# Kernel tuning notes

Measured on AMD Instinct MI355X. Metric: run time of the kernel, lower is better.

Reference implementation:

```python
import jax, jax.numpy as jnp
import numpy as np

B, L, D_MODEL, HEADS, EXP, DEPTH = 2, 2048, 1024, 16, 2, 12
D_EXP = D_MODEL * EXP
D_HEAD = D_EXP // HEADS


def _layernorm(x, g, b, eps=1e-5):
    mu = jnp.mean(x, axis=-1, keepdims=True)
    var = jnp.mean(jnp.square(x - mu), axis=-1, keepdims=True)
    return (x - mu) * jax.lax.rsqrt(var + eps) * g + b


def setup_inputs() -> dict:
    key = jax.random.key(0)
    ks = jax.random.split(key, 4)
    x = jax.random.normal(ks[0], (B, L, D_MODEL), dtype=jnp.float32)
    w_in = jax.random.normal(ks[1], (D_MODEL, 4 * D_EXP), dtype=jnp.float32) * 0.02
    w_out = jax.random.normal(ks[2], (D_EXP, D_MODEL), dtype=jnp.float32) * (0.02 / np.sqrt(2 * DEPTH))
    return {
        "x": x,
        "ln1_g": jnp.ones((D_MODEL,), jnp.float32),
        "ln1_b": jnp.zeros((D_MODEL,), jnp.float32),
        "ln2_g": jnp.ones((D_MODEL,), jnp.float32),
        "ln2_b": jnp.zeros((D_MODEL,), jnp.float32),
        "w_in": w_in,
        "w_out": w_out,
        "smear_factor": jnp.linspace(-6.0, 6.0, HEADS, dtype=jnp.float32),
        "log_scale": jnp.zeros((HEADS,), jnp.float32),
    }


def reference(x, ln1_g, ln1_b, ln2_g, ln2_b, w_in, w_out, smear_factor, log_scale):
    b, l, d = x.shape
    h = smear_factor.shape[0]
    d_exp = w_in.shape[1] // 4
    dh = d_exp // h

    qkvp = _layernorm(x, ln1_g, ln1_b) @ w_in  # [b, l, 4*d_exp]
    q, k, v, p = jnp.split(qkvp, 4, axis=-1)
    # 'b i (h d) -> b h i d'
    to_heads = lambda t: t.reshape(b, l, h, dh).transpose(0, 2, 1, 3)
    q, k, v = to_heads(q), to_heads(k), to_heads(v)

    # smeared keys: k_i <- (1-s)*k_i + s*k_{i-1}  (zero at i=0)
    smear = jax.nn.sigmoid(smear_factor)[None, :, None, None]
    k_prev = jnp.pad(k, ((0, 0), (0, 0), (1, 0), (0, 0)))[:, :, :-1, :]
    k = (1.0 - smear) * k + smear * k_prev

    # ALiBi-style additive mask: slope[h]*j on causal part, -1e10 above diag
    half = h // 2
    slopes = jnp.concatenate([2.0 ** jnp.linspace(0.0, -8.0, half), jnp.zeros((h - half,), jnp.float32)])
    j = jnp.arange(l)
    causal = jnp.where(j[None, :] > j[:, None], jnp.float32(-1e10), jnp.float32(0.0))  # [l, l]
    mask = slopes[:, None, None] * j[None, None, :].astype(jnp.float32) + causal[None, :, :]  # [h, l, l]

    # SDPA with q/s, k/s and default scale 1/sqrt(dh): logits = q k^T / (s^2 sqrt(dh))
    inv = 1.0 / (jnp.exp(2.0 * log_scale)[None, :, None, None] * jnp.sqrt(jnp.float32(dh)))
    logits = jnp.einsum('bhid,bhjd->bhij', q, k) * inv + mask[None]
    attn = jax.nn.softmax(logits, axis=-1)
    o = jnp.einsum('bhij,bhjd->bhid', attn, v)
    o = o.transpose(0, 2, 1, 3).reshape(b, l, h * dh)  # 'b h i d -> b i (h d)'

    out = (jax.nn.silu(p) * o) @ w_out
    return _layernorm(out, ln2_g, ln2_b)
```

## Files before the change

### kernel.cpp

```cpp
#include <hip/hip_runtime.h>

typedef unsigned short u16;
typedef __attribute__((ext_vector_type(8))) short bf16x8;
typedef __attribute__((ext_vector_type(8))) unsigned short u16x8;
typedef __attribute__((ext_vector_type(4))) float f32x4;

#define L_SEQ 2048
#define NTOK 4096
#define DMODEL 1024
#define DEXP 2048
#define NH 16
#define DH 128

__device__ __forceinline__ u16 f2bf(float f) {
    unsigned u = __float_as_uint(f);
    unsigned r = (u + 0x7FFFu + ((u >> 16) & 1u)) >> 16;
    return (u16)r;
}
__device__ __forceinline__ float bf2f(u16 h) {
    return __uint_as_float(((unsigned)h) << 16);
}

__device__ __forceinline__ void gl_lds16(const u16* g, u16* l) {
    __builtin_amdgcn_global_load_lds((const __attribute__((address_space(1))) void*)g,
                                     (__attribute__((address_space(3))) void*)l, 16, 0, 0);
}

__global__ void conv_transpose(const float* __restrict__ in, u16* __restrict__ out, int R, int C) {
    __shared__ unsigned tile[32][33];
    int c0 = blockIdx.x * 32, r0 = blockIdx.y * 32;
    int tx = threadIdx.x, ty = threadIdx.y;
    for (int j = 0; j < 32; j += 8)
        tile[ty + j][tx] = (unsigned)f2bf(in[(size_t)(r0 + ty + j) * C + c0 + tx]);
    __syncthreads();
    for (int j = 0; j < 32; j += 8)
        out[(size_t)(c0 + ty + j) * R + r0 + tx] = (u16)tile[tx][ty + j];
}

__global__ __launch_bounds__(256) void ln_fwd(const float* __restrict__ x, const float* __restrict__ g,
                                              const float* __restrict__ bta, void* __restrict__ outp,
                                              int out_bf16) {
    int row = blockIdx.x;
    int t = threadIdx.x;
    const float* xr = x + (size_t)row * DMODEL;
    float4 xv = *(const float4*)&xr[t * 4];
    float s = xv.x + xv.y + xv.z + xv.w;
    float s2 = xv.x * xv.x + xv.y * xv.y + xv.z * xv.z + xv.w * xv.w;
    for (int off = 32; off >= 1; off >>= 1) {
        s += __shfl_xor(s, off);
        s2 += __shfl_xor(s2, off);
    }
    __shared__ float red[10];
    int w = t >> 6;
    if ((t & 63) == 0) { red[w] = s; red[4 + w] = s2; }
    __syncthreads();
    if (t == 0) {
        red[8] = red[0] + red[1] + red[2] + red[3];
        red[9] = red[4] + red[5] + red[6] + red[7];
    }
    __syncthreads();
    float mu = red[8] * (1.0f / DMODEL);
    float var = red[9] * (1.0f / DMODEL) - mu * mu;
    float rstd = rsqrtf(var + 1e-5f);
    float vals[4] = {xv.x, xv.y, xv.z, xv.w};
    for (int e = 0; e < 4; e++) {
        int c = t * 4 + e;
        float y = (vals[e] - mu) * rstd * g[c] + bta[c];
        if (out_bf16) ((u16*)outp)[(size_t)row * DMODEL + c] = f2bf(y);
        else          ((float*)outp)[(size_t)row * DMODEL + c] = y;
    }
}

__device__ __forceinline__ void store_out(u16* C, size_t idx, float v) { C[idx] = f2bf(v); }
__device__ __forceinline__ void store_out(float* C, size_t idx, float v) { C[idx] = v; }

template <typename OutT>
__global__ __launch_bounds__(256) void gemm_bt(const u16* __restrict__ A, const u16* __restrict__ BT,
                                               OutT* __restrict__ C, int M, int N, int K) {
    __shared__ u16 a_s[2][4096];
    __shared__ u16 b_s[2][4096];
    int tid = threadIdx.x;
    unsigned NX = gridDim.x;
    unsigned lin = blockIdx.x + NX * blockIdx.y;
    unsigned per = NX >> 3;
    unsigned xcd = lin & 7, t = lin >> 3;
    unsigned n_p = xcd * per + (t % per);
    unsigned m_p = t / per;
    int m0 = m_p * 128, n0 = n_p * 128;
    int w = tid >> 6, lane = tid & 63, quad = lane >> 4, ln = lane & 15;
    int wr = (w >> 1) * 64, wc = (w & 1) * 64;
    f32x4 zero4 = {0.f, 0.f, 0.f, 0.f};
    f32x4 acc[4][4];
    for (int r = 0; r < 4; r++)
        for (int c = 0; c < 4; c++) acc[r][c] = zero4;

    int lrow = lane >> 2;
    int lseg = ((lane & 3) ^ ((lrow >> 1) & 3)) * 8;
    int qsw = (quad ^ ((ln >> 1) & 3)) * 8;
    const u16* Ag0 = A + (size_t)(m0 + 32 * w + lrow) * K + lseg;
    const u16* Ag1 = Ag0 + (size_t)16 * K;
    const u16* Bg0 = BT + (size_t)(n0 + 32 * w + lrow) * K + lseg;
    const u16* Bg1 = Bg0 + (size_t)16 * K;
    int lo0 = (2 * w) * 512, lo1 = (2 * w + 1) * 512;

    gl_lds16(Ag0, &a_s[0][lo0]);
    gl_lds16(Ag1, &a_s[0][lo1]);
    gl_lds16(Bg0, &b_s[0][lo0]);
    gl_lds16(Bg1, &b_s[0][lo1]);
    __syncthreads();

    int cur = 0;
    for (int k0 = 0; k0 < K; k0 += 32) {
        if (k0 + 32 < K) {
            int nb = cur ^ 1;
            gl_lds16(Ag0 + k0 + 32, &a_s[nb][lo0]);
            gl_lds16(Ag1 + k0 + 32, &a_s[nb][lo1]);
            gl_lds16(Bg0 + k0 + 32, &b_s[nb][lo0]);
            gl_lds16(Bg1 + k0 + 32, &b_s[nb][lo1]);
        }
        bf16x8 af[4], bfr[4];
        for (int r = 0; r < 4; r++) af[r]  = *(const bf16x8*)&a_s[cur][(wr + r * 16 + ln) * 32 + qsw];
        for (int c = 0; c < 4; c++) bfr[c] = *(const bf16x8*)&b_s[cur][(wc + c * 16 + ln) * 32 + qsw];
        __builtin_amdgcn_s_setprio(1);
        for (int r = 0; r < 4; r++)
            for (int c = 0; c < 4; c++)
                acc[r][c] = __builtin_amdgcn_mfma_f32_16x16x32_bf16(af[r], bfr[c], acc[r][c], 0, 0, 0);
        __builtin_amdgcn_s_setprio(0);
        __syncthreads();
        cur ^= 1;
    }
    for (int r = 0; r < 4; r++)
        for (int c = 0; c < 4; c++)
            for (int e = 0; e < 4; e++) {
                int row = m0 + wr + r * 16 + quad * 4 + e;
                int col = n0 + wc + c * 16 + ln;
                store_out(C, (size_t)row * N + col, acc[r][c][e]);
            }
}

__global__ __launch_bounds__(256) void gemm_bt64(const u16* __restrict__ A, const u16* __restrict__ BT,
                                                 float* __restrict__ C, int M, int N, int K) {
    __shared__ u16 a_s[2][2048];
    __shared__ u16 b_s[2][4096];
    int tid = threadIdx.x;
    unsigned NX = gridDim.x;
    unsigned lin = blockIdx.x + NX * blockIdx.y;
    unsigned per = NX >> 3;
    unsigned xcd = lin & 7, t = lin >> 3;
    unsigned n_p = xcd * per + (t % per);
    unsigned m_p = t / per;
    int m0 = m_p * 64, n0 = n_p * 128;
    int w = tid >> 6, lane = tid & 63, quad = lane >> 4, ln = lane & 15;
    int wc = w * 32;
    f32x4 zero4 = {0.f, 0.f, 0.f, 0.f};
    f32x4 acc[4][2];
    for (int r = 0; r < 4; r++)
        for (int c = 0; c < 2; c++) acc[r][c] = zero4;

    int lrow = lane >> 2;
    int lseg = ((lane & 3) ^ ((lrow >> 1) & 3)) * 8;
    int qsw = (quad ^ ((ln >> 1) & 3)) * 8;
    const u16* Ag  = A + (size_t)(m0 + 16 * w + lrow) * K + lseg;
    const u16* Bg0 = BT + (size_t)(n0 + 32 * w + lrow) * K + lseg;
    const u16* Bg1 = Bg0 + (size_t)16 * K;
    int la = w * 512;
    int lb0 = (2 * w) * 512, lb1 = (2 * w + 1) * 512;

    gl_lds16(Ag, &a_s[0][la]);
    gl_lds16(Bg0, &b_s[0][lb0]);
    gl_lds16(Bg1, &b_s[0][lb1]);
    __syncthreads();

    int cur = 0;
    for (int k0 = 0; k0 < K; k0 += 32) {
        if (k0 + 32 < K) {
            int nb = cur ^ 1;
            gl_lds16(Ag + k0 + 32, &a_s[nb][la]);
            gl_lds16(Bg0 + k0 + 32, &b_s[nb][lb0]);
            gl_lds16(Bg1 + k0 + 32, &b_s[nb][lb1]);
        }
        bf16x8 af[4], bfr[2];
        for (int r = 0; r < 4; r++) af[r]  = *(const bf16x8*)&a_s[cur][(r * 16 + ln) * 32 + qsw];
        for (int c = 0; c < 2; c++) bfr[c] = *(const bf16x8*)&b_s[cur][(wc + c * 16 + ln) * 32 + qsw];
        __builtin_amdgcn_s_setprio(1);
        for (int r = 0; r < 4; r++)
            for (int c = 0; c < 2; c++)
                acc[r][c] = __builtin_amdgcn_mfma_f32_16x16x32_bf16(af[r], bfr[c], acc[r][c], 0, 0, 0);
        __builtin_amdgcn_s_setprio(0);
        __syncthreads();
        cur ^= 1;
    }
    for (int r = 0; r < 4; r++)
        for (int c = 0; c < 2; c++)
            for (int e = 0; e < 4; e++) {
                int row = m0 + r * 16 + quad * 4 + e;
                int col = n0 + wc + c * 16 + ln;
                C[(size_t)row * N + col] = acc[r][c][e];
            }
}

__global__ __launch_bounds__(256) void smear_kernel(const u16* __restrict__ qkvp,
                                                    const float* __restrict__ smear_f,
                                                    u16* __restrict__ k_sm) {
    int gid = blockIdx.x * 256 + threadIdx.x;
    int base = gid * 8;
    int bl = base >> 11;
    int c = base & 2047;
    int h = c >> 7;
    int d = c & 127;
    int l = bl & (L_SEQ - 1);
    int bb = bl >> 11;
    float s = 1.0f / (1.0f + __expf(-smear_f[h]));
    u16x8 cur = *(const u16x8*)&qkvp[(size_t)bl * 8192 + 2048 + c];
    u16x8 prv = {0, 0, 0, 0, 0, 0, 0, 0};
    if (l > 0) prv = *(const u16x8*)&qkvp[(size_t)(bl - 1) * 8192 + 2048 + c];
    u16x8 outv;
    for (int u = 0; u < 8; u++) {
        float kc = bf2f(cur[u]);
        float kp = bf2f(prv[u]);
        outv[u] = f2bf((1.0f - s) * kc + s * kp);
    }
    *(u16x8*)&k_sm[(((size_t)(bb * 16 + h)) * L_SEQ + l) * DH + d] = outv;
}

__global__ void vT_kernel(const u16* __restrict__ qkvp, u16* __restrict__ v_t) {
    __shared__ unsigned tile[32][33];
    int l0 = blockIdx.x * 32, d0 = blockIdx.y * 32;
    int bh = blockIdx.z;
    int bb = bh >> 4, h = bh & 15;
    int tx = threadIdx.x, ty = threadIdx.y;
    size_t tokb = (size_t)bb * L_SEQ;
    for (int j = 0; j < 32; j += 8)
        tile[ty + j][tx] = (unsigned)qkvp[(tokb + l0 + ty + j) * 8192 + 4096 + h * DH + d0 + tx];
    __syncthreads();
    for (int j = 0; j < 32; j += 8)
        v_t[((size_t)bh * DH + d0 + ty + j) * L_SEQ + l0 + tx] = (u16)tile[tx][ty + j];
}

__global__ __launch_bounds__(256) void attn_kernel(const u16* __restrict__ qkvp,
                                                   const u16* __restrict__ k_sm,
                                                   const u16* __restrict__ v_t,
                                                   u16* __restrict__ ag2,
                                                   const float* __restrict__ log_scale) {
    __shared__ u16 k_s[16384];
    __shared__ u16 vt_s[16384];
    __shared__ u16 p_s[4608];
    int tid = threadIdx.x;
    unsigned lin = blockIdx.x + 16u * blockIdx.y;
    unsigned xcd = lin & 7, tt = lin >> 3;
    int bh = (int)(xcd * 4 + (tt & 3));
    int pair = (int)(tt >> 2);
    int bb = bh >> 4, h = bh & 15;
    int w = tid >> 6, lane = tid & 63, quad = lane >> 4, ln = lane & 15;
    size_t tokb = (size_t)bb * L_SEQ;

    const float LOG2E = 1.44269504f;
    float inv = 1.0f / (__expf(2.0f * log_scale[h]) * sqrtf((float)DH));
    float scl = inv * LOG2E;
    float slope2 = ((h < 8) ? exp2f(-8.0f * (float)h / 7.0f) : 0.0f) * LOG2E;

    int lrow = lane >> 2, lcol = lane & 3;
    int lsw8 = (lcol ^ ((lrow >> 1) & 3)) * 8;
    int qsw = (quad ^ ((ln >> 1) & 3)) * 8;
    f32x4 zero4 = {0.f, 0.f, 0.f, 0.f};
    u16* pw = &p_s[w * 1152];
    const short ONE_BF = (short)0x3F80;
    bf16x8 ones = {ONE_BF, ONE_BF, ONE_BF, ONE_BF, ONE_BF, ONE_BF, ONE_BF, ONE_BF};

    for (int sidx = 0; sidx < 2; sidx++) {
        int ib = sidx == 0 ? (31 - pair) : pair;
        int i0 = ib * 64;
        int si = i0 + w * 16;
        int iq = si + ln;

        bf16x8 qf[4];
        for (int kt = 0; kt < 4; kt++)
            qf[kt] = *(const bf16x8*)&qkvp[(tokb + si + ln) * 8192 + h * DH + kt * 32 + quad * 8];

        float mshift = -1e30f;
        float astep = slope2 * 64.0f;
        f32x4 o_acc[8], l_acc;
        for (int dt = 0; dt < 8; dt++) o_acc[dt] = zero4;
        l_acc = zero4;

        float adt0[4][4];
        for (int ct = 0; ct < 4; ct++)
            for (int r = 0; r < 4; r++)
                adt0[ct][r] = slope2 * (float)(ct * 16 + quad * 4 + r);

        const u16* kg[4];
        for (int g = 0; g < 4; g++)
            kg[g] = k_sm + ((size_t)bh * L_SEQ + g * 16 + lrow) * DH + w * 32 + lsw8;
        const u16* vg[4];
        int vloff[4];
        for (int q = 0; q < 4; q++) {
            int c = w * 4 + q;
            int jt = c >> 3, dg = c & 7;
            vg[q] = v_t + ((size_t)bh * DH + dg * 16 + lrow) * L_SEQ + jt * 32 + lsw8;
            vloff[q] = jt * 4096 + dg * 512;
        }

        for (int g = 0; g < 4; g++) { gl_lds16(kg[g], &k_s[w * 2048 + g * 512]); kg[g] += 64 * DH; }
        for (int q = 0; q < 4; q++) { gl_lds16(vg[q], &vt_s[vloff[q]]); vg[q] += 64; }
        __syncthreads();

        int cur = 0;
        for (int j0 = 0; j0 <= i0; j0 += 64) {
            if (j0 + 64 <= i0) {
                int nb = (cur ^ 1) * 8192;
                for (int g = 0; g < 4; g++) { gl_lds16(kg[g], &k_s[nb + w * 2048 + g * 512]); kg[g] += 64 * DH; }
                for (int q = 0; q < 4; q++) { gl_lds16(vg[q], &vt_s[nb + vloff[q]]); vg[q] += 64; }
            }
            const u16* kb = &k_s[cur * 8192];
            const u16* vb = &vt_s[cur * 8192];

            f32x4 sc[4];
            for (int ct = 0; ct < 4; ct++) sc[ct] = zero4;
            __builtin_amdgcn_s_setprio(1);
            for (int kt = 0; kt < 4; kt++)
                for (int ct = 0; ct < 4; ct++) {
                    bf16x8 bfr = *(const bf16x8*)&kb[kt * 2048 + (ct * 16 + ln) * 32 + qsw];
                    sc[ct] = __builtin_amdgcn_mfma_f32_16x16x32_bf16(bfr, qf[kt], sc[ct], 0, 0, 0);
                }
            __builtin_amdgcn_s_setprio(0);

            bool full = (j0 + 63 <= si);
            float s2[4][4];
            for (int ct = 0; ct < 4; ct++)
                for (int r = 0; r < 4; r++) {
                    float v = fmaf(sc[ct][r], scl, adt0[ct][r]);
                    if (!full) {
                        int j = j0 + ct * 16 + quad * 4 + r;
                        if (j > iq) v = -3.0e38f;
                    }
                    s2[ct][r] = v;
                }
            float x0 = fmaxf(fmaxf(s2[0][0], s2[0][1]), s2[0][2]);
            float x1 = fmaxf(fmaxf(s2[0][3], s2[1][0]), s2[1][1]);
            float x2 = fmaxf(fmaxf(s2[1][2], s2[1][3]), s2[2][0]);
            float x3 = fmaxf(fmaxf(s2[2][1], s2[2][2]), s2[2][3]);
            float x4 = fmaxf(fmaxf(s2[3][0], s2[3][1]), s2[3][2]);
            float y0 = fmaxf(fmaxf(x0, x1), x2);
            float y1 = fmaxf(fmaxf(x3, x4), s2[3][3]);
            float mr = fmaxf(y0, y1);
            mr = fmaxf(mr, __shfl_xor(mr, 16));
            mr = fmaxf(mr, __shfl_xor(mr, 32));
            float msh_old = mshift - astep;
            float mnew = fmaxf(msh_old, mr);
            float alpha = exp2f(msh_old - mnew);
            mshift = mnew;

            for (int ct = 0; ct < 4; ct++) {
                float p0 = exp2f(s2[ct][0] - mnew);
                float p1 = exp2f(s2[ct][1] - mnew);
                float p2 = exp2f(s2[ct][2] - mnew);
                float p3 = exp2f(s2[ct][3] - mnew);
                unsigned d0 = __builtin_amdgcn_perm(__float_as_uint(p1), __float_as_uint(p0), 0x07060302u);
                unsigned d1 = __builtin_amdgcn_perm(__float_as_uint(p3), __float_as_uint(p2), 0x07060302u);
                uint2 dd; dd.x = d0; dd.y = d1;
                *(uint2*)&pw[ln * 72 + ct * 16 + quad * 4] = dd;
            }

            if (__any(alpha != 1.0f)) {
                float av[4];
                for (int e = 0; e < 4; e++) av[e] = __shfl(alpha, quad * 20 + e);
                for (int dt = 0; dt < 8; dt++) {
                    f32x4 o = o_acc[dt];
                    for (int e = 0; e < 4; e++) o[e] *= av[e];
                    o_acc[dt] = o;
                }
                for (int e = 0; e < 4; e++) l_acc[e] *= av[e];
            }
            asm volatile("s_waitcnt lgkmcnt(0)" ::: "memory");
            __builtin_amdgcn_s_setprio(1);
            for (int ks = 0; ks < 2; ks++) {
                bf16x8 pa = *(const bf16x8*)&pw[ln * 72 + ks * 32 + quad * 8];
                l_acc = __builtin_amdgcn_mfma_f32_16x16x32_bf16(pa, ones, l_acc, 0, 0, 0);
                for (int dt = 0; dt < 8; dt++) {
                    bf16x8 vf = *(const bf16x8*)&vb[ks * 4096 + (dt * 16 + ln) * 32 + qsw];
                    o_acc[dt] = __builtin_amdgcn_mfma_f32_16x16x32_bf16(pa, vf, o_acc[dt], 0, 0, 0);
                }
            }
            __builtin_amdgcn_s_setprio(0);
            __syncthreads();
            cur ^= 1;
        }

        float rinv[4];
        for (int r = 0; r < 4; r++) rinv[r] = __builtin_amdgcn_rcpf(l_acc[r]);
        for (int dt = 0; dt < 8; dt++)
            for (int r = 0; r < 4; r++) {
                int i = si + quad * 4 + r;
                int dcol = dt * 16 + ln;
                float o = o_acc[dt][r] * rinv[r];
                float pv = bf2f(qkvp[(tokb + i) * 8192 + 6144 + h * DH + dcol]);
                float gate = pv * __builtin_amdgcn_rcpf(1.0f + exp2f(-pv * LOG2E));
                ag2[(tokb + i) * 2048 + h * DH + dcol] = f2bf(gate * o);
            }
    }
}

extern "C" void kernel_launch(void* const* d_in, const int* in_sizes, int n_in,
                              void* d_out, int out_size, void* d_ws, size_t ws_size,
                              hipStream_t stream) {
    const float* x       = (const float*)d_in[0];
    const float* ln1_g   = (const float*)d_in[1];
    const float* ln1_b   = (const float*)d_in[2];
    const float* ln2_g   = (const float*)d_in[3];
    const float* ln2_b   = (const float*)d_in[4];
    const float* w_in    = (const float*)d_in[5];
    const float* w_out   = (const float*)d_in[6];
    const float* smear_f = (const float*)d_in[7];
    const float* logsc   = (const float*)d_in[8];
    float* out = (float*)d_out;
    char* ws = (char*)d_ws;

    u16* w_inT   = (u16*)(ws + 0);
    u16* w_outT  = (u16*)(ws + (size_t)16777216);
    u16* lnA     = (u16*)(ws + (size_t)20971520);
    u16* qkvp    = (u16*)(ws + (size_t)29360128);
    u16* k_sm    = (u16*)(ws + (size_t)96468992);
    u16* ag2     = (u16*)(ws + (size_t)113246208);
    float* out_pre = (float*)(ws + (size_t)96468992);
    u16* v_t     = (u16*)(ws + 0);

    dim3 b32x8(32, 8);
    conv_transpose<<<dim3(8192 / 32, 1024 / 32), b32x8, 0, stream>>>(w_in, w_inT, 1024, 8192);
    conv_transpose<<<dim3(1024 / 32, 2048 / 32), b32x8, 0, stream>>>(w_out, w_outT, 2048, 1024);
    ln_fwd<<<NTOK, 256, 0, stream>>>(x, ln1_g, ln1_b, (void*)lnA, 1);
    gemm_bt<u16><<<dim3(8192 / 128, 4096 / 128), 256, 0, stream>>>(lnA, w_inT, qkvp, NTOK, 8192, 1024);
    smear_kernel<<<4096, 256, 0, stream>>>(qkvp, smear_f, k_sm);
    vT_kernel<<<dim3(L_SEQ / 32, DH / 32, 32), b32x8, 0, stream>>>(qkvp, v_t);
    attn_kernel<<<dim3(16, 32), 256, 0, stream>>>(qkvp, k_sm, v_t, ag2, logsc);
    gemm_bt64<<<dim3(1024 / 128, 4096 / 64), 256, 0, stream>>>(ag2, w_outT, out_pre, NTOK, 1024, 2048);
    ln_fwd<<<NTOK, 256, 0, stream>>>(out_pre, ln2_g, ln2_b, (void*)out, 0);
}
```

Measured before the change: 346.0 us.

## Replace input-projection GEMM with 256x256 tiled 8-wave phased pipeline kernel

Replaces the 128x128 double-buffered input projection GEMM with a 256x256-tile, 512-thread kernel. The kernel splits each K-step of 64 into four quadrant phases. Each phase issues the asynchronous global-to-LDS load for a future half-tile, so loads overlap MFMA work under explicit barriers and vmcnt waits. The larger tile raises arithmetic intensity and data reuse. The costs are 128KB of LDS per block, fewer blocks in the grid (512), and fragile hand-managed waitcnt ordering.

```diff
diff --git a/kernel.cpp b/kernel.cpp
--- a/kernel.cpp
+++ b/kernel.cpp
@@ -71,71 +71,118 @@
     }
 }
 
-__device__ __forceinline__ void store_out(u16* C, size_t idx, float v) { C[idx] = f2bf(v); }
-__device__ __forceinline__ void store_out(float* C, size_t idx, float v) { C[idx] = v; }
-
-template <typename OutT>
-__global__ __launch_bounds__(256) void gemm_bt(const u16* __restrict__ A, const u16* __restrict__ BT,
-                                               OutT* __restrict__ C, int M, int N, int K) {
-    __shared__ u16 a_s[2][4096];
-    __shared__ u16 b_s[2][4096];
+__global__ __launch_bounds__(512, 2) void gemm_8ph(const u16* __restrict__ A, const u16* __restrict__ BT,
+                                                   u16* __restrict__ C, int M, int N, int K) {
+    __shared__ u16 a_s[32768];
+    __shared__ u16 b_s[32768];
     int tid = threadIdx.x;
-    unsigned NX = gridDim.x;
-    unsigned lin = blockIdx.x + NX * blockIdx.y;
-    unsigned per = NX >> 3;
-    unsigned xcd = lin & 7, t = lin >> 3;
-    unsigned n_p = xcd * per + (t % per);
-    unsigned m_p = t / per;
-    int m0 = m_p * 128, n0 = n_p * 128;
     int w = tid >> 6, lane = tid & 63, quad = lane >> 4, ln = lane & 15;
-    int wr = (w >> 1) * 64, wc = (w & 1) * 64;
+    int lsw = ln & 7;
+    int awrow = (w >> 2) * 64 + ln;
+    int bwcol = (w & 3) * 32 + ln;
+
+    unsigned lin = blockIdx.x + gridDim.x * blockIdx.y;
+    unsigned per = gridDim.x >> 3;
+    unsigned xcd = lin & 7, tt = lin >> 3;
+    unsigned n_p = xcd * per + (tt % per);
+    unsigned m_p = tt / per;
+    int m0 = m_p * 256, n0 = n_p * 256;
+
+    const u16 *Ah0[2], *Ah1[2], *Bh0[2], *Bh1[2];
+    int ldoff[2];
+#pragma unroll
+    for (int j = 0; j < 2; j++) {
+        int s = j * 512 + tid;
+        int row = s >> 3, seg = s & 7;
+        int sw = seg ^ (row & 7);
+        Ah0[j] = A + (size_t)(m0 + row) * K + sw * 8;
+        Ah1[j] = A + (size_t)(m0 + 128 + row) * K + sw * 8;
+        Bh0[j] = BT + (size_t)(n0 + row) * K + sw * 8;
+        Bh1[j] = BT + (size_t)(n0 + 128 + row) * K + sw * 8;
+        ldoff[j] = (j * 512 + w * 64) * 8;
+    }
+
     f32x4 zero4 = {0.f, 0.f, 0.f, 0.f};
-    f32x4 acc[4][4];
-    for (int r = 0; r < 4; r++)
-        for (int c = 0; c < 4; c++) acc[r][c] = zero4;
-
-    int lrow = lane >> 2;
-    int lseg = ((lane & 3) ^ ((lrow >> 1) & 3)) * 8;
-    int qsw = (quad ^ ((ln >> 1) & 3)) * 8;
-    const u16* Ag0 = A + (size_t)(m0 + 32 * w + lrow) * K + lseg;
-    const u16* Ag1 = Ag0 + (size_t)16 * K;
-    const u16* Bg0 = BT + (size_t)(n0 + 32 * w + lrow) * K + lseg;
-    const u16* Bg1 = Bg0 + (size_t)16 * K;
-    int lo0 = (2 * w) * 512, lo1 = (2 * w + 1) * 512;
-
-    gl_lds16(Ag0, &a_s[0][lo0]);
-    gl_lds16(Ag1, &a_s[0][lo1]);
-    gl_lds16(Bg0, &b_s[0][lo0]);
-    gl_lds16(Bg1, &b_s[0][lo1]);
-    __syncthreads();
-
-    int cur = 0;
-    for (int k0 = 0; k0 < K; k0 += 32) {
-        if (k0 + 32 < K) {
-            int nb = cur ^ 1;
-            gl_lds16(Ag0 + k0 + 32, &a_s[nb][lo0]);
-            gl_lds16(Ag1 + k0 + 32, &a_s[nb][lo1]);
-            gl_lds16(Bg0 + k0 + 32, &b_s[nb][lo0]);
-            gl_lds16(Bg1 + k0 + 32, &b_s[nb][lo1]);
-        }
-        bf16x8 af[4], bfr[4];
-        for (int r = 0; r < 4; r++) af[r]  = *(const bf16x8*)&a_s[cur][(wr + r * 16 + ln) * 32 + qsw];
-        for (int c = 0; c < 4; c++) bfr[c] = *(const bf16x8*)&b_s[cur][(wc + c * 16 + ln) * 32 + qsw];
-        __builtin_amdgcn_s_setprio(1);
-        for (int r = 0; r < 4; r++)
-            for (int c = 0; c < 4; c++)
-                acc[r][c] = __builtin_amdgcn_mfma_f32_16x16x32_bf16(af[r], bfr[c], acc[r][c], 0, 0, 0);
-        __builtin_amdgcn_s_setprio(0);
-        __syncthreads();
-        cur ^= 1;
-    }
-    for (int r = 0; r < 4; r++)
-        for (int c = 0; c < 4; c++)
-            for (int e = 0; e < 4; e++) {
-                int row = m0 + wr + r * 16 + quad * 4 + e;
-                int col = n0 + wc + c * 16 + ln;
-                store_out(C, (size_t)row * N + col, acc[r][c][e]);
-            }
+    f32x4 acc[4][4][2];
+#pragma unroll
+    for (int q = 0; q < 4; q++)
+#pragma unroll
+        for (int fr = 0; fr < 4; fr++)
+#pragma unroll
+            for (int fc = 0; fc < 2; fc++) acc[q][fr][fc] = zero4;
+
+#define G1_STAGE(MS, PTRS, B, H, T)                                                   \
+    do {                                                                              \
+        _Pragma("unroll") for (int j = 0; j < 2; j++)                                 \
+            gl_lds16(PTRS[j] + (size_t)(T) * 64, &MS[((B)*2 + (H)) * 8192 + ldoff[j]]); \
+    } while (0)
+
+#define G1_PHASE(BUF, QM, QN, STAGE_STMT, TAILGATE)                                   \
+    do {                                                                              \
+        bf16x8 af_[4][2], bf_[2][2];                                                  \
+        _Pragma("unroll") for (int fr = 0; fr < 4; fr++)                              \
+        _Pragma("unroll") for (int ks = 0; ks < 2; ks++)                              \
+            af_[fr][ks] = *(const bf16x8*)&a_s[((BUF)*2 + (QM)) * 8192 +              \
+                (awrow + fr * 16) * 64 + (((ks * 4 + quad) ^ lsw) * 8)];              \
+        _Pragma("unroll") for (int fc = 0; fc < 2; fc++)                              \
+        _Pragma("unroll") for (int ks = 0; ks < 2; ks++)                              \
+            bf_[fc][ks] = *(const bf16x8*)&b_s[((BUF)*2 + (QN)) * 8192 +              \
+                (bwcol + fc * 16) * 64 + (((ks * 4 + quad) ^ lsw) * 8)];              \
+        STAGE_STMT;                                                                   \
+        __builtin_amdgcn_s_barrier();                                                 \
+        asm volatile("s_waitcnt lgkmcnt(0)" ::: "memory");                            \
+        __builtin_amdgcn_sched_barrier(0);                                            \
+        __builtin_amdgcn_s_setprio(1);                                                \
+        _Pragma("unroll") for (int fr = 0; fr < 4; fr++)                              \
+        _Pragma("unroll") for (int fc = 0; fc < 2; fc++)                              \
+        _Pragma("unroll") for (int ks = 0; ks < 2; ks++)                              \
+            acc[(QM)*2 + (QN)][fr][fc] = __builtin_amdgcn_mfma_f32_16x16x32_bf16(     \
+                af_[fr][ks], bf_[fc][ks], acc[(QM)*2 + (QN)][fr][fc], 0, 0, 0);       \
+        __builtin_amdgcn_s_setprio(0);                                                \
+        TAILGATE;                                                                     \
+        __builtin_amdgcn_s_barrier();                                                 \
+    } while (0)
+
+    int NT = K >> 6;
+
+    G1_STAGE(a_s, Ah0, 0, 0, 0);
+    G1_STAGE(a_s, Ah1, 0, 1, 0);
+    G1_STAGE(b_s, Bh0, 0, 0, 0);
+    G1_STAGE(b_s, Bh1, 0, 1, 0);
+    G1_STAGE(a_s, Ah0, 1, 0, 1);
+    G1_STAGE(b_s, Bh1, 1, 1, 1);
+    asm volatile("s_waitcnt vmcnt(4)" ::: "memory");
+    __builtin_amdgcn_s_barrier();
+
+    for (int t = 0; t < NT; t++) {
+        int buf = t & 1, nb = buf ^ 1;
+        G1_PHASE(buf, 0, 0, { if (t + 1 < NT) G1_STAGE(a_s, Ah1, nb, 1, t + 1); }, {});
+        G1_PHASE(buf, 0, 1, { if (t + 1 < NT) G1_STAGE(b_s, Bh0, nb, 0, t + 1); }, {});
+        G1_PHASE(buf, 1, 1, { if (t + 2 < NT) G1_STAGE(a_s, Ah0, buf, 0, t + 2); }, {});
+        G1_PHASE(buf, 1, 0, { if (t + 2 < NT) G1_STAGE(b_s, Bh1, buf, 1, t + 2); },
+                 {
+                     if (t + 2 < NT) asm volatile("s_waitcnt vmcnt(4)" ::: "memory");
+                     else            asm volatile("s_waitcnt vmcnt(0)" ::: "memory");
+                 });
+    }
+
+#undef G1_STAGE
+#undef G1_PHASE
+
+#pragma unroll
+    for (int QM = 0; QM < 2; QM++)
+#pragma unroll
+        for (int QN = 0; QN < 2; QN++)
+#pragma unroll
+            for (int fr = 0; fr < 4; fr++)
+#pragma unroll
+                for (int fc = 0; fc < 2; fc++)
+#pragma unroll
+                    for (int e = 0; e < 4; e++) {
+                        int row = m0 + QM * 128 + (w >> 2) * 64 + fr * 16 + quad * 4 + e;
+                        int col = n0 + QN * 128 + (w & 3) * 32 + fc * 16 + ln;
+                        C[(size_t)row * N + col] = f2bf(acc[QM * 2 + QN][fr][fc][e]);
+                    }
 }
 
 __global__ __launch_bounds__(256) void gemm_bt64(const u16* __restrict__ A, const u16* __restrict__ BT,
@@ -428,7 +475,7 @@
     conv_transpose<<<dim3(8192 / 32, 1024 / 32), b32x8, 0, stream>>>(w_in, w_inT, 1024, 8192);
     conv_transpose<<<dim3(1024 / 32, 2048 / 32), b32x8, 0, stream>>>(w_out, w_outT, 2048, 1024);
     ln_fwd<<<NTOK, 256, 0, stream>>>(x, ln1_g, ln1_b, (void*)lnA, 1);
-    gemm_bt<u16><<<dim3(8192 / 128, 4096 / 128), 256, 0, stream>>>(lnA, w_inT, qkvp, NTOK, 8192, 1024);
+    gemm_8ph<<<dim3(8192 / 256, 4096 / 256), 512, 0, stream>>>(lnA, w_inT, qkvp, NTOK, 8192, 1024);
     smear_kernel<<<4096, 256, 0, stream>>>(qkvp, smear_f, k_sm);
     vT_kernel<<<dim3(L_SEQ / 32, DH / 32, 32), b32x8, 0, stream>>>(qkvp, v_t);
     attn_kernel<<<dim3(16, 32), 256, 0, stream>>>(qkvp, k_sm, v_t, ag2, logsc);
```

New measurement: 344.7 us. About the same (-0.4%).
